# Optimization experiments

Hardware: AMD Instinct MI355X
Metric: run time of the kernel (lower is better)

The kernel has to match this reference:

```python
import jax, jax.numpy as jnp
import numpy as np

ALPHA = jnp.full((8,), 0.25, dtype=jnp.float32)  # per-class focal alpha
GAMMA = 2.0
TEMP = 0.07
CIRC_TARGET = 1.0
CIRC_WEIGHT = 0.1
MIN_AGREE = 0.6
W_FOCAL, W_CONTRAST, W_CONSENSUS = 1.0, 0.5, 0.3


def setup_inputs() -> dict:
    key = jax.random.key(0)
    k1, k2, k3, k4, k5 = jax.random.split(key, 5)
    return {
        "logits": jax.random.normal(k1, (32, 8, 256, 256), dtype=jnp.float32),
        "target": jax.random.randint(k2, (32, 256, 256), 0, 8, dtype=jnp.int32),
        "features": jax.random.normal(k3, (1024, 512), dtype=jnp.float32),
        "masks": jax.random.uniform(k4, (32, 3, 256, 256), dtype=jnp.float32),
        "method_preds": jax.random.uniform(k5, (3, 32, 256, 256), dtype=jnp.float32),
    }


def focal_loss(logits, target):
    B, C, H, W = logits.shape
    x = logits.transpose(0, 2, 3, 1).reshape(-1, C)  # [BHW, C]
    t = target.reshape(-1)
    logp = jax.nn.log_softmax(x, axis=-1)
    ce = -jnp.take_along_axis(logp, t[:, None], axis=1)[:, 0]
    p = jnp.exp(-ce)
    focal_w = ALPHA[t] * (1.0 - p) ** GAMMA
    return jnp.mean(focal_w * ce)


def contrastive_loss(features):
    Bf = features.shape[0]
    f = features / jnp.linalg.norm(features, axis=1, keepdims=True)
    sim = (f @ f.T) / TEMP  # [Bf, Bf]
    # default labels = arange(Bf//2) tiled twice -> each sample has exactly one
    # positive: its paired view at index (i + Bf//2) % Bf
    pos_idx = (jnp.arange(Bf) + Bf // 2) % Bf
    pos = sim[jnp.arange(Bf), pos_idx]
    diag = jnp.eye(Bf, dtype=bool)
    # logits row i = {positive_i} U negatives_i = all j != i (single positive case)
    masked = jnp.where(diag, -1e30, sim)
    lse = jax.nn.logsumexp(masked, axis=1)
    return jnp.mean(lse - pos)  # CE with target = the (only) positive


def circularity_loss(masks):
    m = masks[:, 0]  # [B, H, W] core channel
    B = m.shape[0]
    area = jnp.sum(m, axis=(1, 2))
    ex = jnp.sum(jnp.abs(m[:, 1:, :] - m[:, :-1, :]), axis=(1, 2))
    ey = jnp.sum(jnp.abs(m[:, :, 1:] - m[:, :, :-1]), axis=(1, 2))
    per = ex + ey
    circ = 4.0 * np.pi * area / jnp.maximum(per, 1e-12) ** 2
    li = jnp.where((area > 0) & (per > 0), (circ - CIRC_TARGET) ** 2, 0.0)
    return CIRC_WEIGHT * jnp.sum(li) / B


def consensus_loss(method_preds):
    K = method_preds.shape[0]
    total, n = 0.0, 0
    for i in range(K):  # K=3 methods -> 3 pairs (fixed, small)
        for j in range(i + 1, K):
            pi, pj = method_preds[i], method_preds[j]
            inter = jnp.sum(pi * pj)
            union = jnp.sum(pi + pj - pi * pj)
            iou = inter / (union + 1e-6)
            total = total + jax.nn.relu(MIN_AGREE - iou)
            n += 1
    return total / n


def reference(logits, target, features, masks, method_preds):
    return (W_FOCAL * focal_loss(logits, target)
            + W_CONTRAST * contrastive_loss(features)
            + circularity_loss(masks)
            + W_CONSENSUS * consensus_loss(method_preds))
```

## Files before the change

### kernel.cpp

```cpp
#include <hip/hip_runtime.h>
#include <math.h>

#define WS_FOCALP 0
#define WS_CONSP  2048
#define WS_AREAP  14336
#define WS_EXP_   14848
#define WS_EYP_   15360
#define WS_POS    15872
#define WS_PART   16896
#define WS_HI_B   393216
#define WS_LO_B   1441792

typedef __attribute__((ext_vector_type(8))) short bf16x8;
typedef __attribute__((ext_vector_type(4))) float f32x4;

__device__ inline float wave_reduce(float v) {
#pragma unroll
  for (int m = 32; m >= 1; m >>= 1) v += __shfl_xor(v, m);
  return v;
}

__device__ inline unsigned short bf16_rne(float x) {
  union { float f; unsigned u; } v; v.f = x;
  unsigned r = v.u + 0x7FFF + ((v.u >> 16) & 1);
  return (unsigned short)(r >> 16);
}
__device__ inline float bf16_f(unsigned short h) {
  union { unsigned u; float f; } v; v.u = ((unsigned)h) << 16; return v.f;
}

__device__ inline float focal_px(float v0, float v1, float v2, float v3,
                                 float v4, float v5, float v6, float v7, int tt) {
  float mx = fmaxf(fmaxf(fmaxf(v0, v1), fmaxf(v2, v3)),
                   fmaxf(fmaxf(v4, v5), fmaxf(v6, v7)));
  float se = __expf(v0 - mx) + __expf(v1 - mx) + __expf(v2 - mx) + __expf(v3 - mx) +
             __expf(v4 - mx) + __expf(v5 - mx) + __expf(v6 - mx) + __expf(v7 - mx);
  float xt = v0;
  xt = (tt == 1) ? v1 : xt;
  xt = (tt == 2) ? v2 : xt;
  xt = (tt == 3) ? v3 : xt;
  xt = (tt == 4) ? v4 : xt;
  xt = (tt == 5) ? v5 : xt;
  xt = (tt == 6) ? v6 : xt;
  xt = (tt == 7) ? v7 : xt;
  float lp = (xt - mx) - __logf(se);
  float p = __expf(lp);
  float om = 1.0f - p;
  return 0.25f * om * om * (-lp);
}

__global__ __launch_bounds__(256) void mega_kernel(
    const float* __restrict__ logits, const int* __restrict__ target,
    const float* __restrict__ feat, const float* __restrict__ masks,
    const float* __restrict__ preds, float* __restrict__ ws) {
  __shared__ float red[32];
  const int bid = blockIdx.x;
  const int tid = threadIdx.x;
  const int lane = tid & 63;
  const int wid = tid >> 6;

  if (bid < 2048) {
    int t = bid * 256 + tid;
    int p4 = t * 4;
    int b = p4 >> 16;
    int hw = p4 & 65535;
    const float* lb = logits + (b << 19) + hw;
    float4 x0 = *(const float4*)(lb + (0 << 16));
    float4 x1 = *(const float4*)(lb + (1 << 16));
    float4 x2 = *(const float4*)(lb + (2 << 16));
    float4 x3 = *(const float4*)(lb + (3 << 16));
    float4 x4 = *(const float4*)(lb + (4 << 16));
    float4 x5 = *(const float4*)(lb + (5 << 16));
    float4 x6 = *(const float4*)(lb + (6 << 16));
    float4 x7 = *(const float4*)(lb + (7 << 16));
    int4 tg = *(const int4*)(target + p4);
    float acc = 0.0f;
    acc += focal_px(x0.x, x1.x, x2.x, x3.x, x4.x, x5.x, x6.x, x7.x, tg.x);
    acc += focal_px(x0.y, x1.y, x2.y, x3.y, x4.y, x5.y, x6.y, x7.y, tg.y);
    acc += focal_px(x0.z, x1.z, x2.z, x3.z, x4.z, x5.z, x6.z, x7.z, tg.z);
    acc += focal_px(x0.w, x1.w, x2.w, x3.w, x4.w, x5.w, x6.w, x7.w, tg.w);
    float v = wave_reduce(acc);
    if (lane == 0) red[wid] = v;
    __syncthreads();
    if (tid == 0) ws[WS_FOCALP + bid] = red[0] + red[1] + red[2] + red[3];

  } else if (bid < 2560) {
    int bi = bid - 2048;
    int img = bi >> 4;
    int part = bi & 15;
    const float* mS = masks + img * 3 * 65536;
    const float4* m4 = (const float4*)mS;
    float a = 0.0f, ex = 0.0f, ey = 0.0f;
#pragma unroll
    for (int i = 0; i < 4; i++) {
      int v = tid + 256 * i;
      int rl = v >> 6;
      int c4 = v & 63;
      int row = part * 16 + rl;
      float4 val = m4[row * 64 + c4];
      a += val.x + val.y + val.z + val.w;
      ey += fabsf(val.y - val.x) + fabsf(val.z - val.y) + fabsf(val.w - val.z);
      if (c4 > 0) ey += fabsf(val.x - mS[row * 256 + c4 * 4 - 1]);
      if (row > 0) {
        float4 u = m4[(row - 1) * 64 + c4];
        ex += fabsf(val.x - u.x) + fabsf(val.y - u.y) +
              fabsf(val.z - u.z) + fabsf(val.w - u.w);
      }
    }
    float ra = wave_reduce(a);
    float rx = wave_reduce(ex);
    float ry = wave_reduce(ey);
    if (lane == 0) {
      red[wid + 0] = ra; red[wid + 4] = rx; red[wid + 8] = ry;
    }
    __syncthreads();
    if (tid == 0) {
      ws[WS_AREAP + bi] = red[0] + red[1] + red[2] + red[3];
      ws[WS_EXP_ + bi] = red[4] + red[5] + red[6] + red[7];
      ws[WS_EYP_ + bi] = red[8] + red[9] + red[10] + red[11];
    }

  } else if (bid < 4608) {
    int b = bid - 2560;
    int t = b * 256 + tid;
    const float4* q = (const float4*)preds;
    float4 a0 = q[t];
    float4 a1 = q[t + 524288];
    float4 a2 = q[t + 1048576];
    float s0 = a0.x + a0.y + a0.z + a0.w;
    float s1 = a1.x + a1.y + a1.z + a1.w;
    float s2 = a2.x + a2.y + a2.z + a2.w;
    float p01 = a0.x * a1.x + a0.y * a1.y + a0.z * a1.z + a0.w * a1.w;
    float p02 = a0.x * a2.x + a0.y * a2.y + a0.z * a2.z + a0.w * a2.w;
    float p12 = a1.x * a2.x + a1.y * a2.y + a1.z * a2.z + a1.w * a2.w;
    float r0 = wave_reduce(s0);
    float r1 = wave_reduce(s1);
    float r2 = wave_reduce(s2);
    float r3 = wave_reduce(p01);
    float r4 = wave_reduce(p02);
    float r5 = wave_reduce(p12);
    if (lane == 0) {
      red[wid + 0] = r0; red[wid + 4] = r1; red[wid + 8] = r2;
      red[wid + 12] = r3; red[wid + 16] = r4; red[wid + 20] = r5;
    }
    __syncthreads();
    if (tid == 0) {
#pragma unroll
      for (int k = 0; k < 6; k++)
        ws[WS_CONSP + k * 2048 + b] =
            red[k * 4] + red[k * 4 + 1] + red[k * 4 + 2] + red[k * 4 + 3];
    }

  } else {
    int row = (bid - 4608) * 4 + wid;
    const float4* f4 = (const float4*)feat;
    float4 u = f4[row * 128 + lane];
    float4 w = f4[row * 128 + 64 + lane];
    float s = u.x * u.x + u.y * u.y + u.z * u.z + u.w * u.w +
              w.x * w.x + w.y * w.y + w.z * w.z + w.w * w.w;
    s = wave_reduce(s);
    float scale = 3.7796447300922719f / sqrtf(s);
    float g[8] = {u.x * scale, u.y * scale, u.z * scale, u.w * scale,
                  w.x * scale, w.y * scale, w.z * scale, w.w * scale};
    unsigned short h[8];
    unsigned short l[8];
#pragma unroll
    for (int i = 0; i < 8; i++) {
      h[i] = bf16_rne(g[i]);
      l[i] = bf16_rne(g[i] - bf16_f(h[i]));
    }
    char* hb = (char*)ws + WS_HI_B + row * 1024;
    char* lb = (char*)ws + WS_LO_B + row * 1024;
    *(ushort4*)(hb + lane * 8) = make_ushort4(h[0], h[1], h[2], h[3]);
    *(ushort4*)(hb + 512 + lane * 8) = make_ushort4(h[4], h[5], h[6], h[7]);
    *(ushort4*)(lb + lane * 8) = make_ushort4(l[0], l[1], l[2], l[3]);
    *(ushort4*)(lb + 512 + lane * 8) = make_ushort4(l[4], l[5], l[6], l[7]);
  }
}

__global__ __launch_bounds__(256) void sim_kernel(float* __restrict__ ws) {
  const int tid = threadIdx.x;
  const int lane = tid & 63;
  const int wid = tid >> 6;
  const int rt = blockIdx.x >> 4, ct = blockIdx.x & 15;
  const int wr = wid >> 1, wc = wid & 1;
  const int l15 = lane & 15;
  const int hi8 = lane >> 4;
  const char* HI = (const char*)ws + WS_HI_B;
  const char* LO = (const char*)ws + WS_LO_B;
  const int ar = rt * 64 + wr * 32 + l15;
  const int bc = ct * 64 + wc * 32 + l15;
  const int kb16 = hi8 * 16;

  f32x4 acc[2][2];
#pragma unroll
  for (int r = 0; r < 2; r++)
#pragma unroll
    for (int c = 0; c < 2; c++) acc[r][c] = (f32x4){0.f, 0.f, 0.f, 0.f};

#pragma unroll 4
  for (int kb = 0; kb < 16; kb++) {
    int ko = kb * 64 + kb16;
    bf16x8 ah[2], al[2], bh[2], bl[2];
#pragma unroll
    for (int r = 0; r < 2; r++) {
      ah[r] = *(const bf16x8*)(HI + (ar + r * 16) * 1024 + ko);
      al[r] = *(const bf16x8*)(LO + (ar + r * 16) * 1024 + ko);
    }
#pragma unroll
    for (int c = 0; c < 2; c++) {
      bh[c] = *(const bf16x8*)(HI + (bc + c * 16) * 1024 + ko);
      bl[c] = *(const bf16x8*)(LO + (bc + c * 16) * 1024 + ko);
    }
#pragma unroll
    for (int r = 0; r < 2; r++)
#pragma unroll
      for (int c = 0; c < 2; c++) {
        acc[r][c] = __builtin_amdgcn_mfma_f32_16x16x32_bf16(ah[r], bh[c], acc[r][c], 0, 0, 0);
        acc[r][c] = __builtin_amdgcn_mfma_f32_16x16x32_bf16(ah[r], bl[c], acc[r][c], 0, 0, 0);
        acc[r][c] = __builtin_amdgcn_mfma_f32_16x16x32_bf16(al[r], bh[c], acc[r][c], 0, 0, 0);
      }
  }

  float2* part = (float2*)(ws + WS_PART);
#pragma unroll
  for (int r = 0; r < 2; r++)
#pragma unroll
    for (int q = 0; q < 4; q++) {
      int row = rt * 64 + wr * 32 + r * 16 + hi8 * 4 + q;
      int pc = (row + 512) & 1023;
      float m = -3e38f;
      float v[2];
#pragma unroll
      for (int c = 0; c < 2; c++) {
        int col = ct * 64 + wc * 32 + c * 16 + l15;
        float x = acc[r][c][q];
        if (col == pc) ws[WS_POS + row] = x;
        if (col == row) x = -1e30f;
        v[c] = x;
        m = fmaxf(m, x);
      }
      float s = __expf(v[0] - m) + __expf(v[1] - m);
#pragma unroll
      for (int d = 1; d < 16; d <<= 1) {
        float mo = __shfl_xor(m, d), so = __shfl_xor(s, d);
        float nm = fmaxf(m, mo);
        s = s * __expf(m - nm) + so * __expf(mo - nm);
        m = nm;
      }
      if (l15 == 0) part[row * 32 + ct * 2 + wc] = make_float2(m, s);
    }
}

__global__ __launch_bounds__(1024) void final_kernel(float* __restrict__ ws,
                                                     float* __restrict__ out) {
  __shared__ float red[16][8];
  __shared__ float li_s[32];
  int r = threadIdx.x;
  int lane = r & 63, wid = r >> 6;

  float v[8];
  const float2* part = (const float2*)(ws + WS_PART);
  float M = -1e30f, S = 0.0f;
#pragma unroll
  for (int ctl = 0; ctl < 32; ctl++) {
    float2 p = part[r * 32 + ctl];
    float nm = fmaxf(M, p.x);
    S = S * __expf(M - nm) + p.y * __expf(p.x - nm);
    M = nm;
  }
  v[0] = (M + __logf(S)) - ws[WS_POS + r];
  v[1] = ws[WS_FOCALP + r] + ws[WS_FOCALP + r + 1024];
#pragma unroll
  for (int k = 0; k < 6; k++) {
    const float* p = ws + WS_CONSP + k * 2048;
    v[2 + k] = p[r] + p[r + 1024];
  }
#pragma unroll
  for (int k = 0; k < 8; k++) {
    v[k] = wave_reduce(v[k]);
    if (lane == 0) red[wid][k] = v[k];
  }

  if (r < 512) {
    float a = ws[WS_AREAP + r];
    float ex = ws[WS_EXP_ + r];
    float ey = ws[WS_EYP_ + r];
#pragma unroll
    for (int d = 1; d < 16; d <<= 1) {
      a += __shfl_xor(a, d);
      ex += __shfl_xor(ex, d);
      ey += __shfl_xor(ey, d);
    }
    if ((r & 15) == 0) {
      float per = ex + ey;
      float dd = fmaxf(per, 1e-12f);
      float c = 12.566370614359172f * a / (dd * dd);
      li_s[r >> 4] = (a > 0.0f && per > 0.0f) ? (c - 1.0f) * (c - 1.0f) : 0.0f;
    }
  }
  __syncthreads();

  if (r == 0) {
    float tot[8];
#pragma unroll
    for (int k = 0; k < 8; k++) {
      float t = 0.0f;
#pragma unroll
      for (int i = 0; i < 16; i++) t += red[i][k];
      tot[k] = t;
    }
    float circ = 0.0f;
#pragma unroll
    for (int i = 0; i < 32; i++) circ += li_s[i];
    circ = 0.1f * circ / 32.0f;

    float contr = tot[0] / 1024.0f;
    float focal = tot[1] / 2097152.0f;

    float S0 = tot[2], S1 = tot[3], S2 = tot[4];
    float P01 = tot[5], P02 = tot[6], P12 = tot[7];
    float co = 0.0f;
    co += fmaxf(0.6f - P01 / (S0 + S1 - P01 + 1e-6f), 0.0f);
    co += fmaxf(0.6f - P02 / (S0 + S2 - P02 + 1e-6f), 0.0f);
    co += fmaxf(0.6f - P12 / (S1 + S2 - P12 + 1e-6f), 0.0f);
    co *= (1.0f / 3.0f);

    out[0] = focal + 0.5f * contr + circ + 0.3f * co;
  }
}

extern "C" void kernel_launch(void* const* d_in, const int* in_sizes, int n_in,
                              void* d_out, int out_size, void* d_ws, size_t ws_size,
                              hipStream_t stream) {
  const float* logits = (const float*)d_in[0];
  const int* target = (const int*)d_in[1];
  const float* feat = (const float*)d_in[2];
  const float* masks = (const float*)d_in[3];
  const float* preds = (const float*)d_in[4];
  float* ws = (float*)d_ws;
  float* out = (float*)d_out;

  mega_kernel<<<4864, 256, 0, stream>>>(logits, target, feat, masks, preds, ws);
  sim_kernel<<<256, 256, 0, stream>>>(ws);
  final_kernel<<<1, 1024, 0, stream>>>(ws, out);
}
```

Measured before the change: 57.13 us.

## Split feature prep out and overlap MFMA similarity with streaming reductions

Feature normalization and bf16 hi/lo splitting move into a small prep kernel, and the features are stored in an MFMA fragment-tiled layout so each lane reads one contiguous 16-byte chunk per k-block. The similarity GEMM blocks run as the first 512 blocks of the large fused streaming kernel, so the tensor-core work overlaps with the bandwidth-bound focal, circularity and consensus reductions instead of running as a separate serialized launch. Each GEMM block now covers a smaller 32x64 tile, which doubles the block count and reduces data reuse per block. The goal is to hide the GEMM's latency behind the memory-bound work, at the cost of one extra small launch ahead of the fused kernel.

Result: faster. 47.20 us (-17.4%).

```diff
diff --git a/kernel.cpp b/kernel.cpp
--- a/kernel.cpp
+++ b/kernel.cpp
@@ -49,18 +49,118 @@
   return 0.25f * om * om * (-lp);
 }
 
-__global__ __launch_bounds__(256) void mega_kernel(
+__global__ __launch_bounds__(256) void prep_kernel(const float* __restrict__ feat,
+                                                   float* __restrict__ ws) {
+  const int tid = threadIdx.x;
+  const int lane = tid & 63;
+  const int wid = tid >> 6;
+  int row = blockIdx.x * 4 + wid;
+  const float4* f4 = (const float4*)feat;
+  float4 u = f4[row * 128 + lane];
+  float4 w = f4[row * 128 + 64 + lane];
+  float s = u.x * u.x + u.y * u.y + u.z * u.z + u.w * u.w +
+            w.x * w.x + w.y * w.y + w.z * w.z + w.w * w.w;
+  s = wave_reduce(s);
+  float scale = 3.7796447300922719f / sqrtf(s);
+  float g[8] = {u.x * scale, u.y * scale, u.z * scale, u.w * scale,
+                w.x * scale, w.y * scale, w.z * scale, w.w * scale};
+  unsigned short h[8];
+  unsigned short l[8];
+#pragma unroll
+  for (int i = 0; i < 8; i++) {
+    h[i] = bf16_rne(g[i]);
+    l[i] = bf16_rne(g[i] - bf16_f(h[i]));
+  }
+  const int rg = row >> 4, r15 = row & 15;
+  int k0 = lane * 4;
+  int k1 = 256 + lane * 4;
+  int off0 = (rg * 16 + (k0 >> 5)) * 1024 + (((k0 >> 3) & 3) * 16 + r15) * 16 + (k0 & 7) * 2;
+  int off1 = (rg * 16 + (k1 >> 5)) * 1024 + (((k1 >> 3) & 3) * 16 + r15) * 16 + (k1 & 7) * 2;
+  char* hb = (char*)ws + WS_HI_B;
+  char* lb = (char*)ws + WS_LO_B;
+  *(ushort4*)(hb + off0) = make_ushort4(h[0], h[1], h[2], h[3]);
+  *(ushort4*)(hb + off1) = make_ushort4(h[4], h[5], h[6], h[7]);
+  *(ushort4*)(lb + off0) = make_ushort4(l[0], l[1], l[2], l[3]);
+  *(ushort4*)(lb + off1) = make_ushort4(l[4], l[5], l[6], l[7]);
+}
+
+__global__ __launch_bounds__(256) void fused_kernel(
     const float* __restrict__ logits, const int* __restrict__ target,
-    const float* __restrict__ feat, const float* __restrict__ masks,
-    const float* __restrict__ preds, float* __restrict__ ws) {
+    const float* __restrict__ masks, const float* __restrict__ preds,
+    float* __restrict__ ws) {
   __shared__ float red[32];
   const int bid = blockIdx.x;
   const int tid = threadIdx.x;
   const int lane = tid & 63;
   const int wid = tid >> 6;
 
-  if (bid < 2048) {
-    int t = bid * 256 + tid;
+  if (bid < 512) {
+    const int rt = bid >> 4;
+    const int ct = bid & 15;
+    const int wr = wid >> 1, wc = wid & 1;
+    const int l15 = lane & 15;
+    const int hi8 = lane >> 4;
+    const char* HI = (const char*)ws + WS_HI_B;
+    const char* LO = (const char*)ws + WS_LO_B;
+    const int rga = rt * 2 + wr;
+    const int rgb = ct * 4 + wc * 2;
+    const int lb16 = lane * 16;
+
+    f32x4 acc0 = {0.f, 0.f, 0.f, 0.f};
+    f32x4 acc1 = {0.f, 0.f, 0.f, 0.f};
+
+#pragma unroll 2
+    for (int kb = 0; kb < 16; kb++) {
+      const char* pA = HI + (rga * 16 + kb) * 1024 + lb16;
+      const char* qA = LO + (rga * 16 + kb) * 1024 + lb16;
+      const char* pB0 = HI + (rgb * 16 + kb) * 1024 + lb16;
+      const char* qB0 = LO + (rgb * 16 + kb) * 1024 + lb16;
+      const char* pB1 = HI + ((rgb + 1) * 16 + kb) * 1024 + lb16;
+      const char* qB1 = LO + ((rgb + 1) * 16 + kb) * 1024 + lb16;
+      bf16x8 ah = *(const bf16x8*)pA;
+      bf16x8 al = *(const bf16x8*)qA;
+      bf16x8 bh0 = *(const bf16x8*)pB0;
+      bf16x8 bl0 = *(const bf16x8*)qB0;
+      bf16x8 bh1 = *(const bf16x8*)pB1;
+      bf16x8 bl1 = *(const bf16x8*)qB1;
+      acc0 = __builtin_amdgcn_mfma_f32_16x16x32_bf16(ah, bh0, acc0, 0, 0, 0);
+      acc1 = __builtin_amdgcn_mfma_f32_16x16x32_bf16(ah, bh1, acc1, 0, 0, 0);
+      acc0 = __builtin_amdgcn_mfma_f32_16x16x32_bf16(ah, bl0, acc0, 0, 0, 0);
+      acc1 = __builtin_amdgcn_mfma_f32_16x16x32_bf16(ah, bl1, acc1, 0, 0, 0);
+      acc0 = __builtin_amdgcn_mfma_f32_16x16x32_bf16(al, bh0, acc0, 0, 0, 0);
+      acc1 = __builtin_amdgcn_mfma_f32_16x16x32_bf16(al, bh1, acc1, 0, 0, 0);
+    }
+
+    float2* part = (float2*)(ws + WS_PART);
+    int c0 = ct * 64 + wc * 32 + l15;
+    int c1 = c0 + 16;
+#pragma unroll
+    for (int q = 0; q < 4; q++) {
+      int row = rt * 32 + wr * 16 + hi8 * 4 + q;
+      int pc = (row + 512) & 1023;
+      float v0 = acc0[q], v1 = acc1[q];
+      if (c0 == pc) ws[WS_POS + row] = v0;
+      if (c1 == pc) ws[WS_POS + row] = v1;
+      if (c0 == row) v0 = -1e30f;
+      if (c1 == row) v1 = -1e30f;
+      float m = fmaxf(v0, v1);
+      float s = __expf(v0 - m) + __expf(v1 - m);
+#pragma unroll
+      for (int d = 1; d < 16; d <<= 1) {
+        float mo = __shfl_xor(m, d), so = __shfl_xor(s, d);
+        float nm = fmaxf(m, mo);
+        s = s * __expf(m - nm) + so * __expf(mo - nm);
+        m = nm;
+      }
+      if (l15 == 0) part[row * 32 + ct * 2 + wc] = make_float2(m, s);
+    }
+    return;
+  }
+
+  const int bid2 = bid - 512;
+
+  if (bid2 < 2048) {
+    int t = bid2 * 256 + tid;
     int p4 = t * 4;
     int b = p4 >> 16;
     int hw = p4 & 65535;
@@ -82,10 +182,10 @@
     float v = wave_reduce(acc);
     if (lane == 0) red[wid] = v;
     __syncthreads();
-    if (tid == 0) ws[WS_FOCALP + bid] = red[0] + red[1] + red[2] + red[3];
-
-  } else if (bid < 2560) {
-    int bi = bid - 2048;
+    if (tid == 0) ws[WS_FOCALP + bid2] = red[0] + red[1] + red[2] + red[3];
+
+  } else if (bid2 < 2560) {
+    int bi = bid2 - 2048;
     int img = bi >> 4;
     int part = bi & 15;
     const float* mS = masks + img * 3 * 65536;
@@ -120,8 +220,8 @@
       ws[WS_EYP_ + bi] = red[8] + red[9] + red[10] + red[11];
     }
 
-  } else if (bid < 4608) {
-    int b = bid - 2560;
+  } else {
+    int b = bid2 - 2560;
     int t = b * 256 + tid;
     const float4* q = (const float4*)preds;
     float4 a0 = q[t];
@@ -150,106 +250,7 @@
         ws[WS_CONSP + k * 2048 + b] =
             red[k * 4] + red[k * 4 + 1] + red[k * 4 + 2] + red[k * 4 + 3];
     }
-
-  } else {
-    int row = (bid - 4608) * 4 + wid;
-    const float4* f4 = (const float4*)feat;
-    float4 u = f4[row * 128 + lane];
-    float4 w = f4[row * 128 + 64 + lane];
-    float s = u.x * u.x + u.y * u.y + u.z * u.z + u.w * u.w +
-              w.x * w.x + w.y * w.y + w.z * w.z + w.w * w.w;
-    s = wave_reduce(s);
-    float scale = 3.7796447300922719f / sqrtf(s);
-    float g[8] = {u.x * scale, u.y * scale, u.z * scale, u.w * scale,
-                  w.x * scale, w.y * scale, w.z * scale, w.w * scale};
-    unsigned short h[8];
-    unsigned short l[8];
-#pragma unroll
-    for (int i = 0; i < 8; i++) {
-      h[i] = bf16_rne(g[i]);
-      l[i] = bf16_rne(g[i] - bf16_f(h[i]));
-    }
-    char* hb = (char*)ws + WS_HI_B + row * 1024;
-    char* lb = (char*)ws + WS_LO_B + row * 1024;
-    *(ushort4*)(hb + lane * 8) = make_ushort4(h[0], h[1], h[2], h[3]);
-    *(ushort4*)(hb + 512 + lane * 8) = make_ushort4(h[4], h[5], h[6], h[7]);
-    *(ushort4*)(lb + lane * 8) = make_ushort4(l[0], l[1], l[2], l[3]);
-    *(ushort4*)(lb + 512 + lane * 8) = make_ushort4(l[4], l[5], l[6], l[7]);
-  }
-}
-
-__global__ __launch_bounds__(256) void sim_kernel(float* __restrict__ ws) {
-  const int tid = threadIdx.x;
-  const int lane = tid & 63;
-  const int wid = tid >> 6;
-  const int rt = blockIdx.x >> 4, ct = blockIdx.x & 15;
-  const int wr = wid >> 1, wc = wid & 1;
-  const int l15 = lane & 15;
-  const int hi8 = lane >> 4;
-  const char* HI = (const char*)ws + WS_HI_B;
-  const char* LO = (const char*)ws + WS_LO_B;
-  const int ar = rt * 64 + wr * 32 + l15;
-  const int bc = ct * 64 + wc * 32 + l15;
-  const int kb16 = hi8 * 16;
-
-  f32x4 acc[2][2];
-#pragma unroll
-  for (int r = 0; r < 2; r++)
-#pragma unroll
-    for (int c = 0; c < 2; c++) acc[r][c] = (f32x4){0.f, 0.f, 0.f, 0.f};
-
-#pragma unroll 4
-  for (int kb = 0; kb < 16; kb++) {
-    int ko = kb * 64 + kb16;
-    bf16x8 ah[2], al[2], bh[2], bl[2];
-#pragma unroll
-    for (int r = 0; r < 2; r++) {
-      ah[r] = *(const bf16x8*)(HI + (ar + r * 16) * 1024 + ko);
-      al[r] = *(const bf16x8*)(LO + (ar + r * 16) * 1024 + ko);
-    }
-#pragma unroll
-    for (int c = 0; c < 2; c++) {
-      bh[c] = *(const bf16x8*)(HI + (bc + c * 16) * 1024 + ko);
-      bl[c] = *(const bf16x8*)(LO + (bc + c * 16) * 1024 + ko);
-    }
-#pragma unroll
-    for (int r = 0; r < 2; r++)
-#pragma unroll
-      for (int c = 0; c < 2; c++) {
-        acc[r][c] = __builtin_amdgcn_mfma_f32_16x16x32_bf16(ah[r], bh[c], acc[r][c], 0, 0, 0);
-        acc[r][c] = __builtin_amdgcn_mfma_f32_16x16x32_bf16(ah[r], bl[c], acc[r][c], 0, 0, 0);
-        acc[r][c] = __builtin_amdgcn_mfma_f32_16x16x32_bf16(al[r], bh[c], acc[r][c], 0, 0, 0);
-      }
-  }
-
-  float2* part = (float2*)(ws + WS_PART);
-#pragma unroll
-  for (int r = 0; r < 2; r++)
-#pragma unroll
-    for (int q = 0; q < 4; q++) {
-      int row = rt * 64 + wr * 32 + r * 16 + hi8 * 4 + q;
-      int pc = (row + 512) & 1023;
-      float m = -3e38f;
-      float v[2];
-#pragma unroll
-      for (int c = 0; c < 2; c++) {
-        int col = ct * 64 + wc * 32 + c * 16 + l15;
-        float x = acc[r][c][q];
-        if (col == pc) ws[WS_POS + row] = x;
-        if (col == row) x = -1e30f;
-        v[c] = x;
-        m = fmaxf(m, x);
-      }
-      float s = __expf(v[0] - m) + __expf(v[1] - m);
-#pragma unroll
-      for (int d = 1; d < 16; d <<= 1) {
-        float mo = __shfl_xor(m, d), so = __shfl_xor(s, d);
-        float nm = fmaxf(m, mo);
-        s = s * __expf(m - nm) + so * __expf(mo - nm);
-        m = nm;
-      }
-      if (l15 == 0) part[row * 32 + ct * 2 + wc] = make_float2(m, s);
-    }
+  }
 }
 
 __global__ __launch_bounds__(1024) void final_kernel(float* __restrict__ ws,
@@ -341,7 +342,7 @@
   float* ws = (float*)d_ws;
   float* out = (float*)d_out;
 
-  mega_kernel<<<4864, 256, 0, stream>>>(logits, target, feat, masks, preds, ws);
-  sim_kernel<<<256, 256, 0, stream>>>(ws);
+  prep_kernel<<<256, 256, 0, stream>>>(feat, ws);
+  fused_kernel<<<5120, 256, 0, stream>>>(logits, target, masks, preds, ws);
   final_kernel<<<1, 1024, 0, stream>>>(ws, out);
 }
```

## Pre-swizzle bf16 feature splits into MFMA fragment layout, use one-wave 64x64 sim tiles

Applied to the files above, without the earlier changes.

The normalisation stage now writes the hi/lo bf16 feature splits in a layout already arranged as 16x16x32 MFMA fragments, so each lane reads one contiguous 16-byte chunk per fragment. The sim kernel changes from four waves each computing a 32x32 sub-tile to a single wave computing the whole 64x64 tile with a 4x4 accumulator array, fully unrolled. This doubles operand reuse per loaded fragment and halves the number of partial logsumexp entries per row. The cost is higher register pressure and only 256 single-wave blocks, which may leave the GPU underoccupied and expose load latency.

Result: slower. 65.14 us (+14.0%).

```diff
diff --git a/kernel.cpp b/kernel.cpp
--- a/kernel.cpp
+++ b/kernel.cpp
@@ -8,11 +8,13 @@
 #define WS_EYP_   15360
 #define WS_POS    15872
 #define WS_PART   16896
-#define WS_HI_B   393216
-#define WS_LO_B   1441792
+#define WS_HI_B   1048576
+#define WS_LO_B   2621440
 
 typedef __attribute__((ext_vector_type(8))) short bf16x8;
 typedef __attribute__((ext_vector_type(4))) float f32x4;
+
+#define MFMA16(a, b, c) __builtin_amdgcn_mfma_f32_16x16x32_bf16((a), (b), (c), 0, 0, 0)
 
 __device__ inline float wave_reduce(float v) {
 #pragma unroll
@@ -169,78 +171,79 @@
       h[i] = bf16_rne(g[i]);
       l[i] = bf16_rne(g[i] - bf16_f(h[i]));
     }
-    char* hb = (char*)ws + WS_HI_B + row * 1024;
-    char* lb = (char*)ws + WS_LO_B + row * 1024;
-    *(ushort4*)(hb + lane * 8) = make_ushort4(h[0], h[1], h[2], h[3]);
-    *(ushort4*)(hb + 512 + lane * 8) = make_ushort4(h[4], h[5], h[6], h[7]);
-    *(ushort4*)(lb + lane * 8) = make_ushort4(l[0], l[1], l[2], l[3]);
-    *(ushort4*)(lb + 512 + lane * 8) = make_ushort4(l[4], l[5], l[6], l[7]);
-  }
-}
-
-__global__ __launch_bounds__(256) void sim_kernel(float* __restrict__ ws) {
-  const int tid = threadIdx.x;
-  const int lane = tid & 63;
-  const int wid = tid >> 6;
+    const int rg = row >> 4, r15 = row & 15;
+    int k0 = lane * 4;
+    int k1 = 256 + lane * 4;
+    int off0 = (rg * 16 + (k0 >> 5)) * 1024 + (((k0 >> 3) & 3) * 16 + r15) * 16 + (k0 & 7) * 2;
+    int off1 = (rg * 16 + (k1 >> 5)) * 1024 + (((k1 >> 3) & 3) * 16 + r15) * 16 + (k1 & 7) * 2;
+    char* hb = (char*)ws + WS_HI_B;
+    char* lb = (char*)ws + WS_LO_B;
+    *(ushort4*)(hb + off0) = make_ushort4(h[0], h[1], h[2], h[3]);
+    *(ushort4*)(hb + off1) = make_ushort4(h[4], h[5], h[6], h[7]);
+    *(ushort4*)(lb + off0) = make_ushort4(l[0], l[1], l[2], l[3]);
+    *(ushort4*)(lb + off1) = make_ushort4(l[4], l[5], l[6], l[7]);
+  }
+}
+
+__global__ __launch_bounds__(64) void sim_kernel(float* __restrict__ ws) {
+  const int lane = threadIdx.x;
   const int rt = blockIdx.x >> 4, ct = blockIdx.x & 15;
-  const int wr = wid >> 1, wc = wid & 1;
   const int l15 = lane & 15;
   const int hi8 = lane >> 4;
   const char* HI = (const char*)ws + WS_HI_B;
   const char* LO = (const char*)ws + WS_LO_B;
-  const int ar = rt * 64 + wr * 32 + l15;
-  const int bc = ct * 64 + wc * 32 + l15;
-  const int kb16 = hi8 * 16;
-
-  f32x4 acc[2][2];
-#pragma unroll
-  for (int r = 0; r < 2; r++)
-#pragma unroll
-    for (int c = 0; c < 2; c++) acc[r][c] = (f32x4){0.f, 0.f, 0.f, 0.f};
-
-#pragma unroll 4
+  const int lb16 = lane * 16;
+
+  f32x4 acc[4][4];
+#pragma unroll
+  for (int r = 0; r < 4; r++)
+#pragma unroll
+    for (int c = 0; c < 4; c++) acc[r][c] = (f32x4){0.f, 0.f, 0.f, 0.f};
+
+#pragma unroll
   for (int kb = 0; kb < 16; kb++) {
-    int ko = kb * 64 + kb16;
-    bf16x8 ah[2], al[2], bh[2], bl[2];
-#pragma unroll
-    for (int r = 0; r < 2; r++) {
-      ah[r] = *(const bf16x8*)(HI + (ar + r * 16) * 1024 + ko);
-      al[r] = *(const bf16x8*)(LO + (ar + r * 16) * 1024 + ko);
-    }
-#pragma unroll
-    for (int c = 0; c < 2; c++) {
-      bh[c] = *(const bf16x8*)(HI + (bc + c * 16) * 1024 + ko);
-      bl[c] = *(const bf16x8*)(LO + (bc + c * 16) * 1024 + ko);
-    }
-#pragma unroll
-    for (int r = 0; r < 2; r++)
-#pragma unroll
-      for (int c = 0; c < 2; c++) {
-        acc[r][c] = __builtin_amdgcn_mfma_f32_16x16x32_bf16(ah[r], bh[c], acc[r][c], 0, 0, 0);
-        acc[r][c] = __builtin_amdgcn_mfma_f32_16x16x32_bf16(ah[r], bl[c], acc[r][c], 0, 0, 0);
-        acc[r][c] = __builtin_amdgcn_mfma_f32_16x16x32_bf16(al[r], bh[c], acc[r][c], 0, 0, 0);
+    bf16x8 ah[4], al[4], bh[4], bl[4];
+#pragma unroll
+    for (int r = 0; r < 4; r++) {
+      ah[r] = *(const bf16x8*)(HI + (rt * 4 + r) * 16384 + kb * 1024 + lb16);
+      al[r] = *(const bf16x8*)(LO + (rt * 4 + r) * 16384 + kb * 1024 + lb16);
+    }
+#pragma unroll
+    for (int c = 0; c < 4; c++) {
+      bh[c] = *(const bf16x8*)(HI + (ct * 4 + c) * 16384 + kb * 1024 + lb16);
+      bl[c] = *(const bf16x8*)(LO + (ct * 4 + c) * 16384 + kb * 1024 + lb16);
+    }
+#pragma unroll
+    for (int r = 0; r < 4; r++)
+#pragma unroll
+      for (int c = 0; c < 4; c++) {
+        acc[r][c] = MFMA16(ah[r], bh[c], acc[r][c]);
+        acc[r][c] = MFMA16(ah[r], bl[c], acc[r][c]);
+        acc[r][c] = MFMA16(al[r], bh[c], acc[r][c]);
       }
   }
 
   float2* part = (float2*)(ws + WS_PART);
 #pragma unroll
-  for (int r = 0; r < 2; r++)
+  for (int r = 0; r < 4; r++)
 #pragma unroll
     for (int q = 0; q < 4; q++) {
-      int row = rt * 64 + wr * 32 + r * 16 + hi8 * 4 + q;
+      int row = rt * 64 + r * 16 + hi8 * 4 + q;
       int pc = (row + 512) & 1023;
       float m = -3e38f;
-      float v[2];
-#pragma unroll
-      for (int c = 0; c < 2; c++) {
-        int col = ct * 64 + wc * 32 + c * 16 + l15;
+      float vv[4];
+#pragma unroll
+      for (int c = 0; c < 4; c++) {
+        int col = ct * 64 + c * 16 + l15;
         float x = acc[r][c][q];
         if (col == pc) ws[WS_POS + row] = x;
         if (col == row) x = -1e30f;
-        v[c] = x;
+        vv[c] = x;
         m = fmaxf(m, x);
       }
-      float s = __expf(v[0] - m) + __expf(v[1] - m);
+      float s = 0.0f;
+#pragma unroll
+      for (int c = 0; c < 4; c++) s += __expf(vv[c] - m);
 #pragma unroll
       for (int d = 1; d < 16; d <<= 1) {
         float mo = __shfl_xor(m, d), so = __shfl_xor(s, d);
@@ -248,7 +251,7 @@
         s = s * __expf(m - nm) + so * __expf(mo - nm);
         m = nm;
       }
-      if (l15 == 0) part[row * 32 + ct * 2 + wc] = make_float2(m, s);
+      if (l15 == 0) part[row * 16 + ct] = make_float2(m, s);
     }
 }
 
@@ -263,8 +266,8 @@
   const float2* part = (const float2*)(ws + WS_PART);
   float M = -1e30f, S = 0.0f;
 #pragma unroll
-  for (int ctl = 0; ctl < 32; ctl++) {
-    float2 p = part[r * 32 + ctl];
+  for (int ctl = 0; ctl < 16; ctl++) {
+    float2 p = part[r * 16 + ctl];
     float nm = fmaxf(M, p.x);
     S = S * __expf(M - nm) + p.y * __expf(p.x - nm);
     M = nm;
@@ -342,6 +345,6 @@
   float* out = (float*)d_out;
 
   mega_kernel<<<4864, 256, 0, stream>>>(logits, target, feat, masks, preds, ws);
-  sim_kernel<<<256, 256, 0, stream>>>(ws);
+  sim_kernel<<<256, 64, 0, stream>>>(ws);
   final_kernel<<<1, 1024, 0, stream>>>(ws, out);
 }
```
